# Kernel tuning notes

Hardware: AMD Instinct MI355X
Metric: run time of the kernel (lower is better)

## Reference

```python
import jax, jax.numpy as jnp
import numpy as np
from jax.scipy.special import i0

B, P = 2, 524288
N = (512, 512)            # uniform frequency grid
M = 4                     # window cutoff m (2M taps per dim)
SIGMA = 2.0
NGRID = tuple(2 * (int(SIGMA * Ni) // 2) for Ni in N)  # oversampled grid (1024, 1024)
BETA = tuple(float(np.pi * (2.0 - 1.0 / (ng / Ni))) for ng, Ni in zip(NGRID, N))


def _phi_hat_1d(Ni, ni, b):
    # Fourier coefficients of the Kaiser-Bessel window, k = -Ni/2 .. Ni/2-1
    k = jnp.arange(-Ni // 2, Ni // 2, dtype=jnp.float32)
    arg = jnp.sqrt(b * b - (2.0 * jnp.pi * k / ni) ** 2)
    return i0(M * arg) / ni


def _window_ft():
    # separable d-dim Fourier coefficient grid, shape [N1, N2] (== window.ft)
    c1 = _phi_hat_1d(N[0], NGRID[0], BETA[0])
    c2 = _phi_hat_1d(N[1], NGRID[1], BETA[1])
    return c1[:, None] * c2[None, :]


def _phi(t, ni, b):
    # Kaiser-Bessel window in time domain, support |t| <= M/ni
    u2 = M * M - (ni * t) ** 2
    u = jnp.sqrt(jnp.maximum(u2, 1e-12))
    return jnp.where(u2 > 0, jnp.sinh(b * u) / (jnp.pi * u), 0.0)


def setup_inputs() -> dict:
    key = jax.random.key(0)
    k1, k2 = jax.random.split(key)
    x = jax.random.uniform(k1, (B, P, 2), jnp.float32, -0.5, 0.5)  # points on torus
    f_hat = jax.random.normal(k2, (B, N[0], N[1], 2), jnp.float32)  # complex as [re,im]
    return {"x": x, "f_hat": f_hat}


def _nfft_forward(x, f_hat):
    # f(x_j) ~= sum_k f_hat[k] exp(-2 pi i <k, x_j>) via window-deconvolved oversampled FFT + local gather
    fh = (f_hat[..., 0] + 1j * f_hat[..., 1]).astype(jnp.complex64)  # [B, N1, N2]
    ft = _window_ft().astype(jnp.float32)
    gh = fh / ft                                                    # deconvolve
    p1 = (NGRID[0] - N[0]) // 2
    p2 = (NGRID[1] - N[1]) // 2
    gh = jnp.pad(gh, ((0, 0), (p1, p1), (p2, p2)))                  # centered zero-pad to n
    g = jnp.fft.fftn(jnp.fft.ifftshift(gh, axes=(-2, -1)), axes=(-2, -1))
    g = g / (NGRID[0] * NGRID[1])                                   # g_l = (1/n) sum_k gh_k e^{-2pi i kl/n}

    offs = jnp.arange(-M + 1, M + 1)                                # [2M]
    ws, idxs = [], []
    for d in range(2):
        nd = NGRID[d]
        xd = x[..., d]                                              # [B, P]
        l0 = jnp.floor(xd * nd).astype(jnp.int32)
        l = l0[..., None] + offs                                    # [B, P, 2M]
        t = xd[..., None] - l.astype(jnp.float32) / nd
        ws.append(_phi(t, nd, BETA[d]))
        idxs.append(jnp.mod(l, nd))

    g_flat = g.reshape(B, NGRID[0] * NGRID[1])
    acc = jnp.zeros((B, P), jnp.complex64)
    for i in range(2 * M):                                          # fixed 2m x 2m taps
        for j in range(2 * M):
            flat = idxs[0][..., i] * NGRID[1] + idxs[1][..., j]     # [B, P]
            gv = jnp.take_along_axis(g_flat, flat, axis=1)
            acc = acc + (ws[0][..., i] * ws[1][..., j]) * gv
    return jnp.stack([acc.real, acc.imag], axis=-1)                 # [B, P, 2]


def reference(x, f_hat):
    return _nfft_forward(x, f_hat)
```

## Files before the change

### kernel.cpp

```cpp
#include <hip/hip_runtime.h>

constexpr int   BATCH = 2;
constexpr int   NPTS  = 524288;
constexpr int   BINS  = 2048;
constexpr int   CAP   = 768;
constexpr float BETA  = 4.71238898038469f;
constexpr float PI_F  = 3.14159265358979f;

typedef float v2f __attribute__((ext_vector_type(2)));

#define PIDX(i) ((i) + ((i) >> 4))

constexpr size_t G_BYTES  = (size_t)BATCH * 1024 * 1024 * sizeof(v2f);
constexpr size_t GCNT_OFF = G_BYTES;
constexpr size_t PERM_OFF = G_BYTES + 8192;

__device__ __forceinline__ float i0f_large(float x) {
    float t = 3.75f / x;
    float p =  0.00392377f;
    p = p * t + -0.01647633f;
    p = p * t +  0.02635537f;
    p = p * t + -0.02057706f;
    p = p * t +  0.00916281f;
    p = p * t + -0.00157565f;
    p = p * t +  0.00225319f;
    p = p * t +  0.01328592f;
    p = p * t +  0.39894228f;
    return __expf(x) * rsqrtf(x) * p;
}

__device__ __forceinline__ int tile_of(v2f xv, int b) {
    int c1 = ((int)floorf(xv.x * 1024.0f)) & 1023;
    int c2 = ((int)floorf(xv.y * 1024.0f)) & 1023;
    return (b << 10) + ((c1 >> 5) << 5) + (c2 >> 5);
}

__device__ __forceinline__ v2f cmul4(v2f a, float4 t) {
    v2f lo = {t.x, t.y}, hi = {t.z, t.w};
    return a.x * lo + a.y * hi;
}
__device__ __forceinline__ v2f irot(v2f b) { return (v2f){-b.y, b.x}; }

__device__ __forceinline__ int digitrev4_10(int f) {
    unsigned r = __brev((unsigned)f) >> 22;
    return (int)(((r & 0x2AAu) >> 1) | ((r & 0x155u) << 1));
}

__device__ __forceinline__ void build_tw4(float4* T, int tid, int nthreads) {
    int off = 0, q = 256, sig = 1;
    #pragma unroll
    for (int st = 0; st < 5; ++st) {
        for (int m = tid; m < 3 * q; m += nthreads) {
            int sec = 0, j = m;
            if (j >= q) { sec++; j -= q; }
            if (j >= q) { sec++; j -= q; }
            float ang = (-2.0f * PI_F / 1024.0f) * (float)((sec + 1) * j * sig);
            float sw, cw;
            __sincosf(ang, &sw, &cw);
            T[off + m] = make_float4(cw, sw, -sw, cw);
        }
        off += 3 * q; q >>= 2; sig <<= 2;
    }
}

__device__ __forceinline__ void bfly4(v2f* s, const float4* T,
                                      int bt, int q, int off) {
    int j    = bt & (q - 1);
    int base = ((bt - j) << 2) + j;
    int p0 = PIDX(base), p1 = PIDX(base + q);
    int p2 = PIDX(base + 2 * q), p3 = PIDX(base + 3 * q);
    v2f a0 = s[p0], a1 = s[p1], a2 = s[p2], a3 = s[p3];
    v2f t0 = a0 + a2, t1 = a0 - a2, t2 = a1 + a3, t3 = a1 - a3;
    v2f r3 = irot(t3);
    s[p0] = t0 + t2;
    s[p1] = cmul4(t1 - r3, T[off + j]);
    s[p2] = cmul4(t0 - t2, T[off + q + j]);
    s[p3] = cmul4(t1 + r3, T[off + 2 * q + j]);
}

__global__ __launch_bounds__(256) void rows_and_bin(const v2f* __restrict__ fh,
                                                    v2f* __restrict__ g,
                                                    const v2f* __restrict__ x,
                                                    int* __restrict__ gcnt,
                                                    float4* __restrict__ perm) {
    __shared__ __align__(16) char smem[25072];
    int tid = threadIdx.x;

    if (blockIdx.x < 1024) {
        if (blockIdx.x == 0) {
            #pragma unroll
            for (int i = 0; i < 8; ++i)
                atomicExch(&gcnt[tid * 8 + i], 0);
        }
        v2f*    s = (v2f*)smem;
        float4* T = (float4*)(smem + 8704);
        int blk = blockIdx.x & 511;
        int b   = blockIdx.x >> 9;
        int row = (blk < 256) ? blk : blk + 512;
        int a1  = (row + 256) & 1023;

        build_tw4(T, tid, 256);

        float k1 = (float)(a1 - 256);
        float w1 = (2.0f * PI_F / 1024.0f) * k1;
        float c1 = i0f_large(4.0f * sqrtf(BETA * BETA - w1 * w1));

        const v2f* fr = fh + ((long)b << 18) + ((long)a1 << 9);

        float w2a = (2.0f * PI_F / 1024.0f) * (float)tid;
        float c2a = i0f_large(4.0f * sqrtf(BETA * BETA - w2a * w2a));
        float w2b = (2.0f * PI_F / 1024.0f) * (float)(tid - 256);
        float c2b = i0f_large(4.0f * sqrtf(BETA * BETA - w2b * w2b));

        v2f A = fr[tid + 256] * (1.0f / (c1 * c2a));
        v2f B = fr[tid]       * (1.0f / (c1 * c2b));

        __syncthreads();

        v2f rB = irot(B);
        s[PIDX(tid)]       = A + B;
        s[PIDX(tid + 256)] = cmul4(A + rB, T[tid]);
        s[PIDX(tid + 512)] = cmul4(A - B,  T[256 + tid]);
        s[PIDX(tid + 768)] = cmul4(A - rB, T[512 + tid]);

        int off = 768, q = 64;
        #pragma unroll
        for (int st = 0; st < 4; ++st) {
            __syncthreads();
            bfly4(s, T, tid, q, off);
            off += 3 * q; q >>= 2;
        }
        __syncthreads();

        v2f* base = g + ((long)b << 20) + ((long)row << 10);
        #pragma unroll
        for (int i = 0; i < 4; ++i) {
            int idx = tid + (i << 8);
            base[idx] = s[PIDX(digitrev4_10(idx))];
        }
    } else {
        int* h = (int*)smem;
        int bblk = blockIdx.x - 1024;
        for (int i = tid; i < BINS; i += 256) h[i] = 0;
        __syncthreads();

        int base = bblk * 4096;
        int tile[16];
        v2f pv[16];
        #pragma unroll
        for (int i = 0; i < 16; ++i) {
            int gid = base + tid + i * 256;
            pv[i]   = x[gid];
            tile[i] = tile_of(pv[i], gid >> 19);
            atomicAdd(&h[tile[i]], 1);
        }
        __syncthreads();

        #pragma unroll
        for (int j = 0; j < 8; ++j) {
            int bi = tid + j * 256;
            int c  = h[bi];
            h[bi]  = c ? atomicAdd(&gcnt[bi], c) : 0;
        }
        __syncthreads();

        #pragma unroll
        for (int i = 0; i < 16; ++i) {
            int gid = base + tid + i * 256;
            int pos = atomicAdd(&h[tile[i]], 1);
            perm[tile[i] * CAP + pos] =
                make_float4(pv[i].x, pv[i].y, __int_as_float(gid), 0.0f);
        }
    }
}

__global__ __launch_bounds__(256) void fft_cols(v2f* __restrict__ g) {
    constexpr int STR = 1092;
    __shared__ v2f    s[4 * STR];
    __shared__ float4 T[1023];
    int b  = blockIdx.y;
    int C0 = blockIdx.x * 4;
    int t  = threadIdx.x;
    int c  = t & 3, L = t >> 2;
    v2f* gb = g + ((long)b << 20);

    build_tw4(T, t, 256);

    v2f E[16];
    #pragma unroll
    for (int m = 0; m < 4; ++m) {
        int r = L + 64 * m;
        E[m] = gb[((long)r << 10) + C0 + c];
    }
    #pragma unroll
    for (int m = 12; m < 16; ++m) {
        int r = L + 64 * m;
        E[m] = gb[((long)r << 10) + C0 + c];
    }
    __syncthreads();

    #pragma unroll
    for (int m = 0; m < 4; ++m) {
        v2f A = E[m], B = E[m + 12];
        v2f rB = irot(B);
        int j = L + 64 * m;
        E[m]      = A + B;
        E[m + 4]  = cmul4(A + rB, T[j]);
        E[m + 8]  = cmul4(A - B,  T[256 + j]);
        E[m + 12] = cmul4(A - rB, T[512 + j]);
    }

    {
        float4 u1 = T[768 + L], u2 = T[768 + 64 + L], u3 = T[768 + 128 + L];
        #pragma unroll
        for (int a = 0; a < 4; ++a) {
            v2f a0 = E[4*a], a1 = E[4*a+1], a2 = E[4*a+2], a3 = E[4*a+3];
            v2f t0 = a0 + a2, t1 = a0 - a2, t2 = a1 + a3, t3 = a1 - a3;
            v2f r3 = irot(t3);
            E[4*a]   = t0 + t2;
            E[4*a+1] = cmul4(t1 - r3, u1);
            E[4*a+2] = cmul4(t0 - t2, u2);
            E[4*a+3] = cmul4(t1 + r3, u3);
        }
    }

    v2f* sf = s + c * STR;
    #pragma unroll
    for (int m = 0; m < 16; ++m) sf[PIDX(L + 64 * m)] = E[m];
    __syncthreads();

    #pragma unroll
    for (int rr = 0; rr < 4; ++rr)
        bfly4(sf, T, L + rr * 64, 16, 960);
    __syncthreads();

    v2f C[16];
    int cb = 17 * L;
    #pragma unroll
    for (int j = 0; j < 16; ++j) C[j] = sf[cb + j];

    #pragma unroll
    for (int j = 0; j < 4; ++j) {
        v2f a0 = C[j], a1 = C[j+4], a2 = C[j+8], a3 = C[j+12];
        v2f t0 = a0 + a2, t1 = a0 - a2, t2 = a1 + a3, t3 = a1 - a3;
        v2f r3 = irot(t3);
        C[j]    = t0 + t2;
        C[j+4]  = cmul4(t1 - r3, T[1008 + j]);
        C[j+8]  = cmul4(t0 - t2, T[1012 + j]);
        C[j+12] = cmul4(t1 + r3, T[1016 + j]);
    }
    #pragma unroll
    for (int e = 0; e < 4; ++e) {
        v2f a0 = C[4*e], a1 = C[4*e+1], a2 = C[4*e+2], a3 = C[4*e+3];
        v2f t0 = a0 + a2, t1 = a0 - a2, t2 = a1 + a3, t3 = a1 - a3;
        v2f r3 = irot(t3);
        C[4*e]   = t0 + t2;
        C[4*e+1] = t1 - r3;
        C[4*e+2] = t0 - t2;
        C[4*e+3] = t1 + r3;
    }

    #pragma unroll
    for (int j = 0; j < 16; ++j) {
        int r = digitrev4_10((L << 4) + j);
        gb[((long)r << 10) + C0 + c] = C[j];
    }
}

__global__ __launch_bounds__(256) void gather_binned(const v2f* __restrict__ g,
                                                     const int* __restrict__ gcnt,
                                                     const float4* __restrict__ perm,
                                                     v2f* __restrict__ out) {
    __shared__ v2f patch[37 * 37];
    int tb = blockIdx.x;
    int b  = tb >> 10;
    int tt = tb & 1023;
    int tR = tt >> 5, tC = tt & 31;
    int R0 = (tR << 5) - 2, C0 = (tC << 5) - 2;
    const v2f* gb = g + ((long)b << 20);

    for (int p = threadIdx.x; p < 37 * 37; p += 256) {
        int pr = p / 37, pc = p - pr * 37;
        int gr = (R0 + pr) & 1023, gc = (C0 + pc) & 1023;
        patch[p] = gb[(gr << 10) + gc];
    }
    __syncthreads();

    int cnt = gcnt[tb];
    if (cnt > CAP) cnt = CAP;
    int off0 = tb * CAP;
    for (int i = (int)threadIdx.x; i < cnt; i += 256) {
        float4 rec = perm[off0 + i];
        int gid = __float_as_int(rec.z);

        float w1[6], w2[6];
        int rr0, cc0;
        {
            float xs = rec.x * 1024.0f;
            float fl = floorf(xs);
            float fr = xs - fl;
            rr0 = (((int)fl) & 1023) - (tR << 5);
            #pragma unroll
            for (int k = 0; k < 6; ++k) {
                float tv = fr - (float)(k - 2);
                float u2 = 16.0f - tv * tv;
                float ir = rsqrtf(u2);
                float z  = BETA * u2 * ir;
                w1[k] = __expf(z) * 0.159154943f * ir;
            }
        }
        {
            float xs = rec.y * 1024.0f;
            float fl = floorf(xs);
            float fr = xs - fl;
            cc0 = (((int)fl) & 1023) - (tC << 5);
            #pragma unroll
            for (int k = 0; k < 6; ++k) {
                float tv = fr - (float)(k - 2);
                float u2 = 16.0f - tv * tv;
                float ir = rsqrtf(u2);
                float z  = BETA * u2 * ir;
                w2[k] = __expf(z) * 0.159154943f * ir;
            }
        }

        v2f acc = {0.0f, 0.0f};
        #pragma unroll
        for (int ii = 0; ii < 6; ++ii) {
            int pbase = (rr0 + ii) * 37 + cc0;
            float wi = w1[ii];
            #pragma unroll
            for (int jj = 0; jj < 6; ++jj)
                acc += (wi * w2[jj]) * patch[pbase + jj];
        }
        out[gid] = acc;
    }
}

extern "C" void kernel_launch(void* const* d_in, const int* in_sizes, int n_in,
                              void* d_out, int out_size, void* d_ws, size_t ws_size,
                              hipStream_t stream) {
    const v2f* x  = (const v2f*)d_in[0];
    const v2f* fh = (const v2f*)d_in[1];
    char* ws = (char*)d_ws;
    v2f*    g    = (v2f*)ws;
    int*    gcnt = (int*)(ws + GCNT_OFF);
    float4* perm = (float4*)(ws + PERM_OFF);

    rows_and_bin<<<dim3(1280), dim3(256), 0, stream>>>(fh, g, x, gcnt, perm);
    fft_cols    <<<dim3(256, BATCH), dim3(256), 0, stream>>>(g);

    gather_binned<<<dim3(BINS), dim3(256), 0, stream>>>(g, gcnt, perm, (v2f*)d_out);
}
```

Before: 115.1 us.

## Transpose row-FFT output so column FFT reads contiguous rows

After: 113.3 us. Within noise of the previous version (-1.5%).

```diff
diff --git a/kernel.cpp b/kernel.cpp
--- a/kernel.cpp
+++ b/kernel.cpp
@@ -11,9 +11,11 @@
 
 #define PIDX(i) ((i) + ((i) >> 4))
 
-constexpr size_t G_BYTES  = (size_t)BATCH * 1024 * 1024 * sizeof(v2f);
-constexpr size_t GCNT_OFF = G_BYTES;
-constexpr size_t PERM_OFF = G_BYTES + 8192;
+constexpr size_t G1_OFF   = 0;
+constexpr size_t GT_OFF   = (size_t)16 << 20;
+constexpr size_t GF_OFF   = 0;
+constexpr size_t GCNT_OFF = (size_t)32 << 20;
+constexpr size_t PERM_OFF = GCNT_OFF + 8192;
 
 __device__ __forceinline__ float i0f_large(float x) {
     float t = 3.75f / x;
@@ -174,100 +176,75 @@
     }
 }
 
-__global__ __launch_bounds__(256) void fft_cols(v2f* __restrict__ g) {
-    constexpr int STR = 1092;
-    __shared__ v2f    s[4 * STR];
-    __shared__ float4 T[1023];
-    int b  = blockIdx.y;
-    int C0 = blockIdx.x * 4;
-    int t  = threadIdx.x;
-    int c  = t & 3, L = t >> 2;
-    v2f* gb = g + ((long)b << 20);
-
-    build_tw4(T, t, 256);
-
-    v2f E[16];
-    #pragma unroll
-    for (int m = 0; m < 4; ++m) {
-        int r = L + 64 * m;
-        E[m] = gb[((long)r << 10) + C0 + c];
-    }
-    #pragma unroll
-    for (int m = 12; m < 16; ++m) {
-        int r = L + 64 * m;
-        E[m] = gb[((long)r << 10) + C0 + c];
+__global__ __launch_bounds__(256) void transpose_g(const v2f* __restrict__ g1,
+                                                   v2f* __restrict__ gT) {
+    __shared__ v2f tile[64][65];
+    int bid = blockIdx.x;
+    int b   = bid >> 7;
+    int t7  = bid & 127;
+    int rg  = t7 >> 4;
+    int cg  = t7 & 15;
+    int r0  = ((rg < 4) ? rg : rg + 8) << 6;
+    int c0  = cg << 6;
+    const v2f* src = g1 + ((long)b << 20);
+    v2f*       dst = gT + ((long)b << 20);
+    int lw = threadIdx.x >> 6;
+    int ll = threadIdx.x & 63;
+
+    #pragma unroll
+    for (int k = 0; k < 16; ++k) {
+        int r = lw + (k << 2);
+        tile[r][ll] = src[((long)(r0 + r) << 10) + c0 + ll];
     }
     __syncthreads();
-
-    #pragma unroll
-    for (int m = 0; m < 4; ++m) {
-        v2f A = E[m], B = E[m + 12];
-        v2f rB = irot(B);
-        int j = L + 64 * m;
-        E[m]      = A + B;
-        E[m + 4]  = cmul4(A + rB, T[j]);
-        E[m + 8]  = cmul4(A - B,  T[256 + j]);
-        E[m + 12] = cmul4(A - rB, T[512 + j]);
-    }
-
-    {
-        float4 u1 = T[768 + L], u2 = T[768 + 64 + L], u3 = T[768 + 128 + L];
-        #pragma unroll
-        for (int a = 0; a < 4; ++a) {
-            v2f a0 = E[4*a], a1 = E[4*a+1], a2 = E[4*a+2], a3 = E[4*a+3];
-            v2f t0 = a0 + a2, t1 = a0 - a2, t2 = a1 + a3, t3 = a1 - a3;
-            v2f r3 = irot(t3);
-            E[4*a]   = t0 + t2;
-            E[4*a+1] = cmul4(t1 - r3, u1);
-            E[4*a+2] = cmul4(t0 - t2, u2);
-            E[4*a+3] = cmul4(t1 + r3, u3);
-        }
-    }
-
-    v2f* sf = s + c * STR;
-    #pragma unroll
-    for (int m = 0; m < 16; ++m) sf[PIDX(L + 64 * m)] = E[m];
+    #pragma unroll
+    for (int k = 0; k < 16; ++k) {
+        int c = lw + (k << 2);
+        dst[((long)(c0 + c) << 10) + r0 + ll] = tile[ll][c];
+    }
+}
+
+__global__ __launch_bounds__(256) void fft_cols2(const v2f* __restrict__ gT,
+                                                 v2f* __restrict__ gF) {
+    __shared__ __align__(16) char smem[25072];
+    v2f*    s = (v2f*)smem;
+    float4* T = (float4*)(smem + 8704);
+    int tid = threadIdx.x;
+    int c   = blockIdx.x;
+    int b   = blockIdx.y;
+
+    build_tw4(T, tid, 256);
+
+    const v2f* row = gT + ((long)b << 20) + ((long)c << 10);
+    v2f A = row[tid];
+    v2f B = row[tid + 768];
+
     __syncthreads();
 
-    #pragma unroll
-    for (int rr = 0; rr < 4; ++rr)
-        bfly4(sf, T, L + rr * 64, 16, 960);
+    v2f rB = irot(B);
+    s[PIDX(tid)]       = A + B;
+    s[PIDX(tid + 256)] = cmul4(A + rB, T[tid]);
+    s[PIDX(tid + 512)] = cmul4(A - B,  T[256 + tid]);
+    s[PIDX(tid + 768)] = cmul4(A - rB, T[512 + tid]);
+
+    int off = 768, q = 64;
+    #pragma unroll
+    for (int st = 0; st < 4; ++st) {
+        __syncthreads();
+        bfly4(s, T, tid, q, off);
+        off += 3 * q; q >>= 2;
+    }
     __syncthreads();
 
-    v2f C[16];
-    int cb = 17 * L;
-    #pragma unroll
-    for (int j = 0; j < 16; ++j) C[j] = sf[cb + j];
-
-    #pragma unroll
-    for (int j = 0; j < 4; ++j) {
-        v2f a0 = C[j], a1 = C[j+4], a2 = C[j+8], a3 = C[j+12];
-        v2f t0 = a0 + a2, t1 = a0 - a2, t2 = a1 + a3, t3 = a1 - a3;
-        v2f r3 = irot(t3);
-        C[j]    = t0 + t2;
-        C[j+4]  = cmul4(t1 - r3, T[1008 + j]);
-        C[j+8]  = cmul4(t0 - t2, T[1012 + j]);
-        C[j+12] = cmul4(t1 + r3, T[1016 + j]);
-    }
-    #pragma unroll
-    for (int e = 0; e < 4; ++e) {
-        v2f a0 = C[4*e], a1 = C[4*e+1], a2 = C[4*e+2], a3 = C[4*e+3];
-        v2f t0 = a0 + a2, t1 = a0 - a2, t2 = a1 + a3, t3 = a1 - a3;
-        v2f r3 = irot(t3);
-        C[4*e]   = t0 + t2;
-        C[4*e+1] = t1 - r3;
-        C[4*e+2] = t0 - t2;
-        C[4*e+3] = t1 + r3;
-    }
-
-    #pragma unroll
-    for (int j = 0; j < 16; ++j) {
-        int r = digitrev4_10((L << 4) + j);
-        gb[((long)r << 10) + C0 + c] = C[j];
-    }
-}
-
-__global__ __launch_bounds__(256) void gather_binned(const v2f* __restrict__ g,
+    v2f* o = gF + ((long)b << 20) + ((long)c << 10);
+    #pragma unroll
+    for (int i = 0; i < 4; ++i) {
+        int idx = tid + (i << 8);
+        o[idx] = s[PIDX(digitrev4_10(idx))];
+    }
+}
+
+__global__ __launch_bounds__(256) void gather_binned(const v2f* __restrict__ gF,
                                                      const int* __restrict__ gcnt,
                                                      const float4* __restrict__ perm,
                                                      v2f* __restrict__ out) {
@@ -277,12 +254,12 @@
     int tt = tb & 1023;
     int tR = tt >> 5, tC = tt & 31;
     int R0 = (tR << 5) - 2, C0 = (tC << 5) - 2;
-    const v2f* gb = g + ((long)b << 20);
+    const v2f* gb = gF + ((long)b << 20);
 
     for (int p = threadIdx.x; p < 37 * 37; p += 256) {
-        int pr = p / 37, pc = p - pr * 37;
-        int gr = (R0 + pr) & 1023, gc = (C0 + pc) & 1023;
-        patch[p] = gb[(gr << 10) + gc];
+        int pa = p / 37, pb = p - pa * 37;
+        int gc = (C0 + pa) & 1023, gr = (R0 + pb) & 1023;
+        patch[p] = gb[(gc << 10) + gr];
     }
     __syncthreads();
 
@@ -326,12 +303,12 @@
 
         v2f acc = {0.0f, 0.0f};
         #pragma unroll
-        for (int ii = 0; ii < 6; ++ii) {
-            int pbase = (rr0 + ii) * 37 + cc0;
-            float wi = w1[ii];
+        for (int jj = 0; jj < 6; ++jj) {
+            int pbase = (cc0 + jj) * 37 + rr0;
+            float wj = w2[jj];
             #pragma unroll
-            for (int jj = 0; jj < 6; ++jj)
-                acc += (wi * w2[jj]) * patch[pbase + jj];
+            for (int ii = 0; ii < 6; ++ii)
+                acc += (wj * w1[ii]) * patch[pbase + ii];
         }
         out[gid] = acc;
     }
@@ -343,12 +320,14 @@
     const v2f* x  = (const v2f*)d_in[0];
     const v2f* fh = (const v2f*)d_in[1];
     char* ws = (char*)d_ws;
-    v2f*    g    = (v2f*)ws;
+    v2f*    g1   = (v2f*)(ws + G1_OFF);
+    v2f*    gT   = (v2f*)(ws + GT_OFF);
+    v2f*    gF   = (v2f*)(ws + GF_OFF);
     int*    gcnt = (int*)(ws + GCNT_OFF);
     float4* perm = (float4*)(ws + PERM_OFF);
 
-    rows_and_bin<<<dim3(1280), dim3(256), 0, stream>>>(fh, g, x, gcnt, perm);
-    fft_cols    <<<dim3(256, BATCH), dim3(256), 0, stream>>>(g);
-
-    gather_binned<<<dim3(BINS), dim3(256), 0, stream>>>(g, gcnt, perm, (v2f*)d_out);
-}
+    rows_and_bin <<<dim3(1280),        dim3(256), 0, stream>>>(fh, g1, x, gcnt, perm);
+    transpose_g  <<<dim3(256),         dim3(256), 0, stream>>>(g1, gT);
+    fft_cols2    <<<dim3(1024, BATCH), dim3(256), 0, stream>>>(gT, gF);
+    gather_binned<<<dim3(BINS),        dim3(256), 0, stream>>>(gF, gcnt, perm, (v2f*)d_out);
+}
```
